# Performance work log

Measured on AMD Instinct MI355X. Metric: run time of the kernel, lower is better.

## Reference

```python
import jax, jax.numpy as jnp
import numpy as np

B, S, D = 4, 2048, 1024
H, HD = 16, 64
TAU = HD ** -0.5
N_MASKED = 256  # last keys masked (padding)


def setup_inputs() -> dict:
    key = jax.random.key(0)
    ks = jax.random.split(key, 8)
    sc = 0.02
    mask = jnp.zeros((B, 1, 1, S), dtype=bool).at[..., S - N_MASKED:].set(True)
    return {
        "q": jax.random.normal(ks[0], (B, S, D), dtype=jnp.float32),
        "k": jax.random.normal(ks[1], (B, S, D), dtype=jnp.float32),
        "v": jax.random.normal(ks[2], (B, S, D), dtype=jnp.float32),
        "mask": mask,
        "Wq": jax.random.normal(ks[3], (D, H * HD), dtype=jnp.float32) * sc,
        "bq": jnp.zeros((H * HD,), dtype=jnp.float32),
        "Wk": jax.random.normal(ks[4], (D, H * HD), dtype=jnp.float32) * sc,
        "bk": jnp.zeros((H * HD,), dtype=jnp.float32),
        "Wv": jax.random.normal(ks[5], (D, H * HD), dtype=jnp.float32) * sc,
        "bv": jnp.zeros((H * HD,), dtype=jnp.float32),
        "Wo": jax.random.normal(ks[6], (H * HD, D), dtype=jnp.float32) * sc,
        "bo": jnp.zeros((D,), dtype=jnp.float32),
    }


def reference(q, k, v, mask, Wq, bq, Wk, bk, Wv, bv, Wo, bo):
    # projections: [..., s, D] -> [..., s, H, HD]
    qh = (q @ Wq + bq).reshape(*q.shape[:-1], H, HD)
    kh = (k @ Wk + bk).reshape(*k.shape[:-1], H, HD)
    vh = (v @ Wv + bv).reshape(*v.shape[:-1], H, HD)
    # scores: [B, H, Q, K]
    attn = jnp.einsum('bqhd,bkhd->bhqk', qh, kh) * TAU
    attn = jnp.where(mask, -jnp.inf, attn)  # masked_fill(mask, -inf)
    # dropout(p=0) before softmax is identity
    p = jax.nn.softmax(attn, axis=-1)
    out = jnp.einsum('bhqk,bkhd->bqhd', p, vh).reshape(*q.shape[:-1], H * HD)
    return out @ Wo + bo  # [B, S, D]
```

## Files before the change

kernel.cpp:

```cpp
#include <hip/hip_runtime.h>
#include <hip/hip_fp16.h>
#include <cstdint>
#include <cstddef>

#define B_  4
#define S_  2048
#define D_  1024
#define H_  16
#define HD_ 64
#define TAU_ 0.125f
#define QSCALE_ 0.18033688011112042f

typedef _Float16 f16;
typedef __attribute__((ext_vector_type(8)))  _Float16 f16x8;
typedef __attribute__((ext_vector_type(4)))  _Float16 f16x4;
typedef __attribute__((ext_vector_type(2)))  __fp16   fp16x2_b;
typedef __attribute__((ext_vector_type(4)))  float    f32x4;
typedef __attribute__((ext_vector_type(16))) float    f32x16;
typedef __attribute__((ext_vector_type(2)))  unsigned u32x2;

__device__ __forceinline__ void gload_lds16(const f16* g, f16* l) {
    __builtin_amdgcn_global_load_lds(
        (const __attribute__((address_space(1))) unsigned int*)g,
        (__attribute__((address_space(3)))       unsigned int*)l,
        16, 0, 0);
}

__device__ __forceinline__ unsigned pkh(float a, float b) {
    fp16x2_b h = __builtin_amdgcn_cvt_pkrtz(a, b);
    return __builtin_bit_cast(unsigned, h);
}

__device__ __forceinline__ float exp2_hw(float x) {
    float r;
    asm("v_exp_f32 %0, %1" : "=v"(r) : "v"(x));
    return r;
}

__device__ __forceinline__ float max3f(float a, float b, float c) {
    float r;
    asm("v_max3_f32 %0, %1, %2, %3" : "=v"(r) : "v"(a), "v"(b), "v"(c));
    return r;
}

__device__ __forceinline__ float pair_max(float x) {
    unsigned xu = __builtin_bit_cast(unsigned, x);
    u32x2 r = __builtin_amdgcn_permlane32_swap(xu, xu, false, false);
    return fmaxf(__builtin_bit_cast(float, r[0]), __builtin_bit_cast(float, r[1]));
}
__device__ __forceinline__ float pair_sum(float x) {
    unsigned xu = __builtin_bit_cast(unsigned, x);
    u32x2 r = __builtin_amdgcn_permlane32_swap(xu, xu, false, false);
    return __builtin_bit_cast(float, r[0]) + __builtin_bit_cast(float, r[1]);
}

__global__ __launch_bounds__(256) void mask_norm_kernel(
    const unsigned char* __restrict__ mp, unsigned char* __restrict__ nm,
    float* __restrict__ mf)
{
    __shared__ int flags[3];
    const int tid = threadIdx.x;
    if (tid < 3) flags[tid] = 0;
    __syncthreads();
    int loc0 = 0, loc1 = 0, loc2 = 0;
    for (int i = 0; i < 32; ++i) {
        int off = tid * 32 + i;
        unsigned char v = mp[off];
        if (v) {
            int m = off & 3;
            if (m == 0) loc0 = 1;
            else if (m == 1) loc1 = 1;
            else loc2 = 1;
        }
    }
    if (loc0) atomicOr(&flags[0], 1);
    if (loc1) atomicOr(&flags[1], 1);
    if (loc2) atomicOr(&flags[2], 1);
    __syncthreads();
    const int mode = flags[1] ? 0 : (flags[2] ? 2 : (flags[0] ? 1 : 0));
    for (int i = 0; i < 32; ++i) {
        int idx = tid * 32 + i;
        unsigned char r;
        if (mode == 0)      r = mp[idx] ? 1 : 0;
        else if (mode == 1) r = ((const int*)mp)[idx] ? 1 : 0;
        else                r = (((const float*)mp)[idx] != 0.f) ? 1 : 0;
        nm[idx] = r;
        mf[idx] = r ? -1e30f : 0.f;
    }
}

__global__ __launch_bounds__(256) void wconv_kernel(
    const float* __restrict__ W0, const float* __restrict__ W1,
    const float* __restrict__ W2, const float* __restrict__ W3,
    f16* __restrict__ Wt)
{
    __shared__ float T[64][65];
    const int z = blockIdx.z;
    const float* W = (z == 0) ? W0 : (z == 1) ? W1 : (z == 2) ? W2 : W3;
    f16* out = Wt + (size_t)z * D_ * D_;
    const int n0 = blockIdx.x * 64, k0 = blockIdx.y * 64;
    const int tid = threadIdx.x;
    for (int j = 0; j < 4; ++j) {
        int idx = j * 256 + tid;
        int r = idx >> 4, c4 = idx & 15;
        float4 v = *(const float4*)&W[(size_t)(k0 + r) * D_ + n0 + c4 * 4];
        T[r][c4 * 4 + 0] = v.x; T[r][c4 * 4 + 1] = v.y;
        T[r][c4 * 4 + 2] = v.z; T[r][c4 * 4 + 3] = v.w;
    }
    __syncthreads();
    for (int j = 0; j < 16; ++j) {
        int idx = j * 256 + tid;
        int nl = idx >> 6, kl = idx & 63;
        out[(size_t)(n0 + nl) * D_ + k0 + kl] = (f16)T[kl][nl];
    }
}

__global__ __launch_bounds__(256) void f32to16_kernel(
    const float* __restrict__ a0, const float* __restrict__ a1,
    const float* __restrict__ a2, f16* __restrict__ o0,
    f16* __restrict__ o1, f16* __restrict__ o2)
{
    const int z = blockIdx.y;
    const float* a = (z == 0) ? a0 : (z == 1) ? a1 : a2;
    f16* o = (z == 0) ? o0 : (z == 1) ? o1 : o2;
    const int N4 = (B_ * S_ * D_) / 4;
    for (int i = blockIdx.x * 256 + threadIdx.x; i < N4; i += gridDim.x * 256) {
        float4 v = ((const float4*)a)[i];
        f16x4 h;
        h[0] = (f16)v.x; h[1] = (f16)v.y; h[2] = (f16)v.z; h[3] = (f16)v.w;
        ((f16x4*)o)[i] = h;
    }
}

template <bool A16>
__device__ __forceinline__ void gemm_body(
    const void* __restrict__ Ap, const f16* __restrict__ Wt,
    const float* __restrict__ bias, void* __restrict__ Cp,
    int m0, int n0, float oscale, int outmode)
{
    __shared__ __align__(16) f16 Al[128 * 64];
    __shared__ __align__(16) f16 Bl[128 * 64];
    const int tid = threadIdx.x, lane = tid & 63, wid = tid >> 6;
    const int wm = (wid >> 1) * 64, wn = (wid & 1) * 64;
    const int g = lane >> 4, c = lane & 15;

    f32x4 acc[4][4] = {};

    for (int kt = 0; kt < 16; ++kt) {
        const int k0 = kt * 64;
        for (int i = 0; i < 4; ++i) {
            int ch  = wid * 4 + i;
            int row = ch * 8 + (lane >> 3);
            int ls  = (lane & 7) ^ (row & 7);
            gload_lds16(Wt + (size_t)(n0 + row) * 1024 + k0 + ls * 8,
                        Bl + ch * 512);
        }
        if (A16) {
            const f16* A = (const f16*)Ap;
            for (int i = 0; i < 4; ++i) {
                int ch  = wid * 4 + i;
                int row = ch * 8 + (lane >> 3);
                int ls  = (lane & 7) ^ (row & 7);
                gload_lds16(A + (size_t)(m0 + row) * 1024 + k0 + ls * 8,
                            Al + ch * 512);
            }
        } else {
            const float* A = (const float*)Ap;
            for (int j = 0; j < 8; ++j) {
                int idx = j * 256 + tid;
                int row = idx >> 4, c4 = idx & 15;
                float4 v = *(const float4*)&A[(size_t)(m0 + row) * 1024 + k0 + c4 * 4];
                f16x4 h;
                h[0] = (f16)v.x; h[1] = (f16)v.y; h[2] = (f16)v.z; h[3] = (f16)v.w;
                int ps = (c4 >> 1) ^ (row & 7);
                *(f16x4*)&Al[row * 64 + ps * 8 + (c4 & 1) * 4] = h;
            }
        }
        __syncthreads();
        for (int kc = 0; kc < 2; ++kc) {
            f16x8 af[4], bf[4];
            for (int mb = 0; mb < 4; ++mb) {
                int row = wm + mb * 16 + c;
                af[mb] = *(const f16x8*)&Al[row * 64 + ((kc * 4 + g) ^ (row & 7)) * 8];
            }
            for (int nb = 0; nb < 4; ++nb) {
                int row = wn + nb * 16 + c;
                bf[nb] = *(const f16x8*)&Bl[row * 64 + ((kc * 4 + g) ^ (row & 7)) * 8];
            }
            for (int mb = 0; mb < 4; ++mb)
                for (int nb = 0; nb < 4; ++nb)
                    acc[mb][nb] = __builtin_amdgcn_mfma_f32_16x16x32_f16(
                        af[mb], bf[nb], acc[mb][nb], 0, 0, 0);
        }
        __syncthreads();
    }
    for (int nb = 0; nb < 4; ++nb) {
        int n = n0 + wn + nb * 16 + c;
        float bv = bias[n];
        for (int mb = 0; mb < 4; ++mb)
            for (int r = 0; r < 4; ++r) {
                int m = m0 + wm + mb * 16 + g * 4 + r;
                float v = (acc[mb][nb][r] + bv) * oscale;
                if (outmode == 1) {
                    ((f16*)Cp)[(((size_t)(m >> 11) * H_ + (n >> 6)) * HD_ + (n & 63)) * S_ + (m & 2047)] = (f16)v;
                } else if (outmode == 0) {
                    ((f16*)Cp)[(size_t)m * 1024 + n] = (f16)v;
                } else {
                    ((float*)Cp)[(size_t)m * 1024 + n] = v;
                }
            }
    }
}

__global__ __launch_bounds__(256) void gemm_qkv16_kernel(
    const f16* __restrict__ qf, const f16* __restrict__ kf,
    const f16* __restrict__ vf, const f16* __restrict__ Wt,
    const float* __restrict__ bq, const float* __restrict__ bk,
    const float* __restrict__ bv, f16* __restrict__ outbase)
{
    const int z = blockIdx.z;
    const f16* A    = (z == 0) ? qf : (z == 1) ? kf : vf;
    const float* bi = (z == 0) ? bq : (z == 1) ? bk : bv;
    gemm_body<true>(A, Wt + (size_t)z * D_ * D_, bi,
                    outbase + (size_t)z * S_ * B_ * D_,
                    blockIdx.x * 128, blockIdx.y * 128,
                    z == 0 ? QSCALE_ : 1.f, z == 2 ? 1 : 0);
}

__global__ __launch_bounds__(256) void gemm_qkv32_kernel(
    const float* __restrict__ q, const float* __restrict__ k,
    const float* __restrict__ v, const f16* __restrict__ Wt,
    const float* __restrict__ bq, const float* __restrict__ bk,
    const float* __restrict__ bv, f16* __restrict__ outbase)
{
    const int z = blockIdx.z;
    const float* A  = (z == 0) ? q  : (z == 1) ? k  : v;
    const float* bi = (z == 0) ? bq : (z == 1) ? bk : bv;
    gemm_body<false>(A, Wt + (size_t)z * D_ * D_, bi,
                     outbase + (size_t)z * S_ * B_ * D_,
                     blockIdx.x * 128, blockIdx.y * 128,
                     z == 0 ? QSCALE_ : 1.f, z == 2 ? 1 : 0);
}

__global__ __launch_bounds__(256) void gemm_out_kernel(
    const f16* __restrict__ Oh, const f16* __restrict__ WtO,
    const float* __restrict__ bo, float* __restrict__ out)
{
    gemm_body<true>(Oh, WtO, bo, out, blockIdx.x * 128, blockIdx.y * 128, 1.f, 2);
}

__global__ __launch_bounds__(256, 2) void attn_kernel(
    const f16* __restrict__ qh, const f16* __restrict__ kh,
    const f16* __restrict__ vt, const unsigned char* __restrict__ maskp,
    const float* __restrict__ maskf, f16* __restrict__ Oh)
{
    __shared__ __align__(16) f16 Kl[2][128 * 64];
    __shared__ __align__(16) f16 VTl[2][64 * 128];
    const int tid = threadIdx.x, lane = tid & 63, wid = tid >> 6;
    const int ql = lane & 31, hi = lane >> 5;
    const int lg = ((blockIdx.x & 7) << 7) + (blockIdx.x >> 3);
    const int h = (lg >> 4) & 15, b = lg >> 8;
    const int q0 = (lg & 15) * 128 + wid * 32;

    const unsigned char* mrow = maskp + (size_t)b * S_;
    const float* mfrow = maskf + (size_t)b * S_;
    const size_t kbase  = (size_t)b * S_ * D_ + (size_t)h * HD_;
    const size_t vtbase = ((size_t)b * H_ + h) * (size_t)HD_ * S_;

    unsigned live = 0, part = 0;
    for (int t = 0; t < 16; ++t) {
        unsigned long long b0 = __ballot(mrow[t * 128 + lane] != 0);
        unsigned long long b1 = __ballot(mrow[t * 128 + 64 + lane] != 0);
        if (b0 != ~0ull || b1 != ~0ull) {
            live |= 1u << t;
            if (b0 | b1) part |= 1u << t;
        }
    }

    f16x8 qf[4];
    {
        const f16* qrow = qh + ((size_t)(b * S_ + q0 + ql) * H_ + h) * HD_;
        #pragma unroll
        for (int dc = 0; dc < 4; ++dc)
            qf[dc] = *(const f16x8*)&qrow[dc * 16 + hi * 8];
    }

    float m_ = -1e30f, l_ = 0.f;
    f32x16 accO[2] = {};

    auto stage = [&](int kv0, int bb) {
        #pragma unroll
        for (int i = 0; i < 4; ++i) {
            int ch  = wid * 4 + i;
            int row = ch * 8 + (lane >> 3);
            int ls  = (lane & 7) ^ (row & 7);
            gload_lds16(kh + kbase + (size_t)(kv0 + row) * D_ + ls * 8,
                        &Kl[bb][ch * 512]);
            int hdr = ch * 4 + (lane >> 4);
            int vs  = (lane & 15) ^ ((hdr & 7) << 1);
            gload_lds16(vt + vtbase + (size_t)hdr * S_ + kv0 + vs * 8,
                        &VTl[bb][ch * 512]);
        }
    };

    if (live) {
        int t = __builtin_ctz(live);
        stage(t * 128, 0);
        __syncthreads();
        int cur = 0;
        for (;;) {
            unsigned rem = live & (0xFFFFFFFEu << t);
            int tn = rem ? __builtin_ctz(rem) : 32;
            if (tn < 32) stage(tn * 128, cur ^ 1);

            const int kv0 = t * 128;
            const f16* Kb = &Kl[cur][0];
            const f16* Vb = &VTl[cur][0];

            f32x16 sacc[4] = {};
            __builtin_amdgcn_s_setprio(1);
            #pragma unroll
            for (int ks = 0; ks < 4; ++ks) {
                const int key = ks * 32 + ql;
                #pragma unroll
                for (int dc = 0; dc < 4; ++dc) {
                    int slot = (dc * 2 + hi) ^ (key & 7);
                    f16x8 kf = *(const f16x8*)&Kb[key * 64 + slot * 8];
                    sacc[ks] = __builtin_amdgcn_mfma_f32_32x32x16_f16(
                        kf, qf[dc], sacc[ks], 0, 0, 0);
                }
            }
            __builtin_amdgcn_s_setprio(0);
            if (part & (1u << t)) {
                #pragma unroll
                for (int ks = 0; ks < 4; ++ks)
                    #pragma unroll
                    for (int r = 0; r < 16; ++r) {
                        int key = kv0 + ks * 32 + (r & 3) + 8 * (r >> 2) + 4 * hi;
                        sacc[ks][r] += mfrow[key];
                    }
            }
            float mx;
            {
                float m0 = max3f(sacc[0][0], sacc[0][1], sacc[0][2]);
                float m1 = max3f(sacc[1][0], sacc[1][1], sacc[1][2]);
                float m2 = max3f(sacc[2][0], sacc[2][1], sacc[2][2]);
                float m3 = max3f(sacc[3][0], sacc[3][1], sacc[3][2]);
                #pragma unroll
                for (int r = 3; r < 15; r += 2) {
                    m0 = max3f(m0, sacc[0][r], sacc[0][r + 1]);
                    m1 = max3f(m1, sacc[1][r], sacc[1][r + 1]);
                    m2 = max3f(m2, sacc[2][r], sacc[2][r + 1]);
                    m3 = max3f(m3, sacc[3][r], sacc[3][r + 1]);
                }
                m0 = fmaxf(m0, sacc[0][15]); m1 = fmaxf(m1, sacc[1][15]);
                m2 = fmaxf(m2, sacc[2][15]); m3 = fmaxf(m3, sacc[3][15]);
                mx = max3f(m0, m1, m2);
                mx = fmaxf(mx, m3);
            }
            mx = pair_max(mx);
            if (__ballot(mx > m_ + 8.f)) {
                float mnew = fmaxf(m_, mx);
                float alpha = exp2_hw(m_ - mnew);
                m_ = mnew;
                l_ *= alpha;
                #pragma unroll
                for (int blk = 0; blk < 2; ++blk)
                    #pragma unroll
                    for (int r = 0; r < 16; ++r) accO[blk][r] *= alpha;
            }
            float ts = 0.f;
            #pragma unroll
            for (int ks = 0; ks < 4; ++ks)
                #pragma unroll
                for (int r = 0; r < 16; ++r) {
                    float p = exp2_hw(sacc[ks][r] - m_);
                    sacc[ks][r] = p;
                    ts += p;
                }
            l_ += pair_sum(ts);

            #pragma unroll
            for (int ks = 0; ks < 4; ++ks) {
                unsigned Pq[4][2];
                #pragma unroll
                for (int j = 0; j < 4; ++j) {
                    Pq[j][0] = pkh(sacc[ks][4 * j + 0], sacc[ks][4 * j + 1]);
                    Pq[j][1] = pkh(sacc[ks][4 * j + 2], sacc[ks][4 * j + 3]);
                }
                #pragma unroll
                for (int kc = 0; kc < 2; ++kc) {
                    union { f16x8 v; unsigned u[4]; } pf;
                    u32x2 s0 = __builtin_amdgcn_permlane32_swap(Pq[2 * kc][0], Pq[2 * kc + 1][0], false, false);
                    u32x2 s1 = __builtin_amdgcn_permlane32_swap(Pq[2 * kc][1], Pq[2 * kc + 1][1], false, false);
                    pf.u[0] = s0[0]; pf.u[2] = s0[1];
                    pf.u[1] = s1[0]; pf.u[3] = s1[1];
                    const int s = ks * 2 + kc;
                    __builtin_amdgcn_s_setprio(1);
                    #pragma unroll
                    for (int blk = 0; blk < 2; ++blk) {
                        int hd = blk * 32 + ql;
                        int slot = (s * 2 + hi) ^ ((hd & 7) << 1);
                        f16x8 vtf = *(const f16x8*)&Vb[hd * 128 + slot * 8];
                        accO[blk] = __builtin_amdgcn_mfma_f32_32x32x16_f16(
                            vtf, pf.v, accO[blk], 0, 0, 0);
                    }
                    __builtin_amdgcn_s_setprio(0);
                }
            }
            __syncthreads();
            cur ^= 1;
            if (tn == 32) break;
            t = tn;
        }
    }
    const float invl = (l_ > 0.f) ? 1.f / l_ : 0.f;
    f16* orow = Oh + ((size_t)(b * S_ + q0 + ql) * H_ + h) * HD_;
    #pragma unroll
    for (int blk = 0; blk < 2; ++blk)
        #pragma unroll
        for (int j = 0; j < 4; ++j) {
            f16x4 o;
            #pragma unroll
            for (int tt = 0; tt < 4; ++tt)
                o[tt] = (f16)(accO[blk][4 * j + tt] * invl);
            *(f16x4*)&orow[blk * 32 + 4 * hi + 8 * j] = o;
        }
}

extern "C" void kernel_launch(void* const* d_in, const int* in_sizes, int n_in,
                              void* d_out, int out_size, void* d_ws, size_t ws_size,
                              hipStream_t stream)
{
    const float* q    = (const float*)d_in[0];
    const float* k    = (const float*)d_in[1];
    const float* v    = (const float*)d_in[2];
    const unsigned char* mask = (const unsigned char*)d_in[3];
    const float* Wq   = (const float*)d_in[4];
    const float* bq   = (const float*)d_in[5];
    const float* Wk   = (const float*)d_in[6];
    const float* bk   = (const float*)d_in[7];
    const float* Wv   = (const float*)d_in[8];
    const float* bv   = (const float*)d_in[9];
    const float* Wo   = (const float*)d_in[10];
    const float* bo   = (const float*)d_in[11];
    float* out        = (float*)d_out;

    char* ws = (char*)d_ws;
    const size_t MB = 1048576;
    f16* Wt  = (f16*)ws;
    f16* qh  = (f16*)(ws + 8 * MB);
    f16* khp = (f16*)(ws + 24 * MB);
    f16* vtp = (f16*)(ws + 40 * MB);
    f16* Ohp = (f16*)(ws + 56 * MB);
    unsigned char* nm = (unsigned char*)(ws + 72 * MB);
    float* mf = (float*)(ws + 72 * MB + 8192);
    f16* qf16 = (f16*)(ws + 76 * MB);
    f16* kf16 = (f16*)(ws + 92 * MB);
    f16* vf16 = (f16*)(ws + 108 * MB);
    const bool use16 = ws_size >= 124 * MB;

    mask_norm_kernel<<<1, 256, 0, stream>>>(mask, nm, mf);
    wconv_kernel<<<dim3(16, 16, 4), 256, 0, stream>>>(Wq, Wk, Wv, Wo, Wt);
    if (use16) {
        f32to16_kernel<<<dim3(1024, 3), 256, 0, stream>>>(q, k, v, qf16, kf16, vf16);
        gemm_qkv16_kernel<<<dim3(64, 8, 3), 256, 0, stream>>>(
            qf16, kf16, vf16, Wt, bq, bk, bv, qh);
    } else {
        gemm_qkv32_kernel<<<dim3(64, 8, 3), 256, 0, stream>>>(
            q, k, v, Wt, bq, bk, bv, qh);
    }
    attn_kernel<<<1024, 256, 0, stream>>>(qh, khp, vtp, nm, mf, Ohp);
    gemm_out_kernel<<<dim3(64, 8), 256, 0, stream>>>(Ohp, Wt + (size_t)3 * D_ * D_, bo, out);
}
```

Baseline: 243.5 us.

## Load fp32 activations directly to LDS and convert in QKV GEMM

Drops the separate fp32-to-fp16 conversion pass over q, k and v. The QKV projection GEMM now loads fp32 activation tiles straight into shared memory with async global-to-LDS copies, using a 16-way XOR swizzle, and converts them to fp16 when reading MFMA fragments. This avoids writing and re-reading about 48 MB of fp16 intermediates and saves a kernel launch. In exchange the A tile doubles in LDS, each tile is converted redundantly by the two wave columns, and more A bytes are read per GEMM tile.

```diff
diff --git a/kernel.cpp b/kernel.cpp
--- a/kernel.cpp
+++ b/kernel.cpp
@@ -19,7 +19,7 @@
 typedef __attribute__((ext_vector_type(16))) float    f32x16;
 typedef __attribute__((ext_vector_type(2)))  unsigned u32x2;
 
-__device__ __forceinline__ void gload_lds16(const f16* g, f16* l) {
+__device__ __forceinline__ void gload_lds16(const void* g, void* l) {
     __builtin_amdgcn_global_load_lds(
         (const __attribute__((address_space(1))) unsigned int*)g,
         (__attribute__((address_space(3)))       unsigned int*)l,
@@ -115,31 +115,22 @@
     }
 }
 
-__global__ __launch_bounds__(256) void f32to16_kernel(
-    const float* __restrict__ a0, const float* __restrict__ a1,
-    const float* __restrict__ a2, f16* __restrict__ o0,
-    f16* __restrict__ o1, f16* __restrict__ o2)
-{
-    const int z = blockIdx.y;
-    const float* a = (z == 0) ? a0 : (z == 1) ? a1 : a2;
-    f16* o = (z == 0) ? o0 : (z == 1) ? o1 : o2;
-    const int N4 = (B_ * S_ * D_) / 4;
-    for (int i = blockIdx.x * 256 + threadIdx.x; i < N4; i += gridDim.x * 256) {
-        float4 v = ((const float4*)a)[i];
-        f16x4 h;
-        h[0] = (f16)v.x; h[1] = (f16)v.y; h[2] = (f16)v.z; h[3] = (f16)v.w;
-        ((f16x4*)o)[i] = h;
-    }
-}
-
-template <bool A16>
-__device__ __forceinline__ void gemm_body(
-    const void* __restrict__ Ap, const f16* __restrict__ Wt,
-    const float* __restrict__ bias, void* __restrict__ Cp,
-    int m0, int n0, float oscale, int outmode)
-{
-    __shared__ __align__(16) f16 Al[128 * 64];
-    __shared__ __align__(16) f16 Bl[128 * 64];
+__global__ __launch_bounds__(256) void gemm_qkvf_kernel(
+    const float* __restrict__ q, const float* __restrict__ k,
+    const float* __restrict__ v, const f16* __restrict__ Wt,
+    const float* __restrict__ bq, const float* __restrict__ bk,
+    const float* __restrict__ bv, f16* __restrict__ outbase)
+{
+    __shared__ __align__(16) float Al[128 * 64];
+    __shared__ __align__(16) f16  Bl[128 * 64];
+    const int z = blockIdx.z;
+    const float* A  = (z == 0) ? q  : (z == 1) ? k  : v;
+    const float* bi = (z == 0) ? bq : (z == 1) ? bk : bv;
+    const f16*  W   = Wt + (size_t)z * D_ * D_;
+    f16* Cp         = outbase + (size_t)z * S_ * B_ * D_;
+    const float oscale = (z == 0) ? QSCALE_ : 1.f;
+    const int outmode  = (z == 2) ? 1 : 0;
+    const int m0 = blockIdx.x * 128, n0 = blockIdx.y * 128;
     const int tid = threadIdx.x, lane = tid & 63, wid = tid >> 6;
     const int wm = (wid >> 1) * 64, wn = (wid & 1) * 64;
     const int g = lane >> 4, c = lane & 15;
@@ -152,29 +143,81 @@
             int ch  = wid * 4 + i;
             int row = ch * 8 + (lane >> 3);
             int ls  = (lane & 7) ^ (row & 7);
-            gload_lds16(Wt + (size_t)(n0 + row) * 1024 + k0 + ls * 8,
+            gload_lds16(W + (size_t)(n0 + row) * 1024 + k0 + ls * 8,
                         Bl + ch * 512);
         }
-        if (A16) {
-            const f16* A = (const f16*)Ap;
-            for (int i = 0; i < 4; ++i) {
-                int ch  = wid * 4 + i;
-                int row = ch * 8 + (lane >> 3);
-                int ls  = (lane & 7) ^ (row & 7);
-                gload_lds16(A + (size_t)(m0 + row) * 1024 + k0 + ls * 8,
-                            Al + ch * 512);
-            }
-        } else {
-            const float* A = (const float*)Ap;
-            for (int j = 0; j < 8; ++j) {
-                int idx = j * 256 + tid;
-                int row = idx >> 4, c4 = idx & 15;
-                float4 v = *(const float4*)&A[(size_t)(m0 + row) * 1024 + k0 + c4 * 4];
-                f16x4 h;
-                h[0] = (f16)v.x; h[1] = (f16)v.y; h[2] = (f16)v.z; h[3] = (f16)v.w;
-                int ps = (c4 >> 1) ^ (row & 7);
-                *(f16x4*)&Al[row * 64 + ps * 8 + (c4 & 1) * 4] = h;
-            }
+        for (int i = 0; i < 8; ++i) {
+            int ch  = wid * 8 + i;
+            int row = ch * 4 + (lane >> 4);
+            int ls  = (lane & 15) ^ (row & 15);
+            gload_lds16(A + (size_t)(m0 + row) * 1024 + k0 + ls * 4,
+                        Al + ch * 256);
+        }
+        __syncthreads();
+        for (int kc = 0; kc < 2; ++kc) {
+            f16x8 af[4], bf[4];
+            for (int mb = 0; mb < 4; ++mb) {
+                int row = wm + mb * 16 + c;
+                int sl  = kc * 8 + g * 2;
+                f32x4 a0 = *(const f32x4*)&Al[row * 64 + ((sl)     ^ (row & 15)) * 4];
+                f32x4 a1 = *(const f32x4*)&Al[row * 64 + ((sl + 1) ^ (row & 15)) * 4];
+                f16x8 hfr;
+                hfr[0] = (f16)a0[0]; hfr[1] = (f16)a0[1];
+                hfr[2] = (f16)a0[2]; hfr[3] = (f16)a0[3];
+                hfr[4] = (f16)a1[0]; hfr[5] = (f16)a1[1];
+                hfr[6] = (f16)a1[2]; hfr[7] = (f16)a1[3];
+                af[mb] = hfr;
+            }
+            for (int nb = 0; nb < 4; ++nb) {
+                int row = wn + nb * 16 + c;
+                bf[nb] = *(const f16x8*)&Bl[row * 64 + ((kc * 4 + g) ^ (row & 7)) * 8];
+            }
+            for (int mb = 0; mb < 4; ++mb)
+                for (int nb = 0; nb < 4; ++nb)
+                    acc[mb][nb] = __builtin_amdgcn_mfma_f32_16x16x32_f16(
+                        af[mb], bf[nb], acc[mb][nb], 0, 0, 0);
+        }
+        __syncthreads();
+    }
+    for (int nb = 0; nb < 4; ++nb) {
+        int n = n0 + wn + nb * 16 + c;
+        float bv2 = bi[n];
+        for (int mb = 0; mb < 4; ++mb)
+            for (int r = 0; r < 4; ++r) {
+                int m = m0 + wm + mb * 16 + g * 4 + r;
+                float val = (acc[mb][nb][r] + bv2) * oscale;
+                if (outmode == 1) {
+                    Cp[(((size_t)(m >> 11) * H_ + (n >> 6)) * HD_ + (n & 63)) * S_ + (m & 2047)] = (f16)val;
+                } else {
+                    Cp[(size_t)m * 1024 + n] = (f16)val;
+                }
+            }
+    }
+}
+
+__global__ __launch_bounds__(256) void gemm_out_kernel(
+    const f16* __restrict__ Oh, const f16* __restrict__ WtO,
+    const float* __restrict__ bo, float* __restrict__ out)
+{
+    __shared__ __align__(16) f16 Al[128 * 64];
+    __shared__ __align__(16) f16 Bl[128 * 64];
+    const int m0 = blockIdx.x * 128, n0 = blockIdx.y * 128;
+    const int tid = threadIdx.x, lane = tid & 63, wid = tid >> 6;
+    const int wm = (wid >> 1) * 64, wn = (wid & 1) * 64;
+    const int g = lane >> 4, c = lane & 15;
+
+    f32x4 acc[4][4] = {};
+
+    for (int kt = 0; kt < 16; ++kt) {
+        const int k0 = kt * 64;
+        for (int i = 0; i < 4; ++i) {
+            int ch  = wid * 4 + i;
+            int row = ch * 8 + (lane >> 3);
+            int ls  = (lane & 7) ^ (row & 7);
+            gload_lds16(WtO + (size_t)(n0 + row) * 1024 + k0 + ls * 8,
+                        Bl + ch * 512);
+            gload_lds16(Oh + (size_t)(m0 + row) * 1024 + k0 + ls * 8,
+                        Al + ch * 512);
         }
         __syncthreads();
         for (int kc = 0; kc < 2; ++kc) {
@@ -196,57 +239,13 @@
     }
     for (int nb = 0; nb < 4; ++nb) {
         int n = n0 + wn + nb * 16 + c;
-        float bv = bias[n];
+        float bv = bo[n];
         for (int mb = 0; mb < 4; ++mb)
             for (int r = 0; r < 4; ++r) {
                 int m = m0 + wm + mb * 16 + g * 4 + r;
-                float v = (acc[mb][nb][r] + bv) * oscale;
-                if (outmode == 1) {
-                    ((f16*)Cp)[(((size_t)(m >> 11) * H_ + (n >> 6)) * HD_ + (n & 63)) * S_ + (m & 2047)] = (f16)v;
-                } else if (outmode == 0) {
-                    ((f16*)Cp)[(size_t)m * 1024 + n] = (f16)v;
-                } else {
-                    ((float*)Cp)[(size_t)m * 1024 + n] = v;
-                }
-            }
-    }
-}
-
-__global__ __launch_bounds__(256) void gemm_qkv16_kernel(
-    const f16* __restrict__ qf, const f16* __restrict__ kf,
-    const f16* __restrict__ vf, const f16* __restrict__ Wt,
-    const float* __restrict__ bq, const float* __restrict__ bk,
-    const float* __restrict__ bv, f16* __restrict__ outbase)
-{
-    const int z = blockIdx.z;
-    const f16* A    = (z == 0) ? qf : (z == 1) ? kf : vf;
-    const float* bi = (z == 0) ? bq : (z == 1) ? bk : bv;
-    gemm_body<true>(A, Wt + (size_t)z * D_ * D_, bi,
-                    outbase + (size_t)z * S_ * B_ * D_,
-                    blockIdx.x * 128, blockIdx.y * 128,
-                    z == 0 ? QSCALE_ : 1.f, z == 2 ? 1 : 0);
-}
-
-__global__ __launch_bounds__(256) void gemm_qkv32_kernel(
-    const float* __restrict__ q, const float* __restrict__ k,
-    const float* __restrict__ v, const f16* __restrict__ Wt,
-    const float* __restrict__ bq, const float* __restrict__ bk,
-    const float* __restrict__ bv, f16* __restrict__ outbase)
-{
-    const int z = blockIdx.z;
-    const float* A  = (z == 0) ? q  : (z == 1) ? k  : v;
-    const float* bi = (z == 0) ? bq : (z == 1) ? bk : bv;
-    gemm_body<false>(A, Wt + (size_t)z * D_ * D_, bi,
-                     outbase + (size_t)z * S_ * B_ * D_,
-                     blockIdx.x * 128, blockIdx.y * 128,
-                     z == 0 ? QSCALE_ : 1.f, z == 2 ? 1 : 0);
-}
-
-__global__ __launch_bounds__(256) void gemm_out_kernel(
-    const f16* __restrict__ Oh, const f16* __restrict__ WtO,
-    const float* __restrict__ bo, float* __restrict__ out)
-{
-    gemm_body<true>(Oh, WtO, bo, out, blockIdx.x * 128, blockIdx.y * 128, 1.f, 2);
+                out[(size_t)m * 1024 + n] = acc[mb][nb][r] + bv;
+            }
+    }
 }
 
 __global__ __launch_bounds__(256, 2) void attn_kernel(
@@ -455,21 +454,10 @@
     f16* Ohp = (f16*)(ws + 56 * MB);
     unsigned char* nm = (unsigned char*)(ws + 72 * MB);
     float* mf = (float*)(ws + 72 * MB + 8192);
-    f16* qf16 = (f16*)(ws + 76 * MB);
-    f16* kf16 = (f16*)(ws + 92 * MB);
-    f16* vf16 = (f16*)(ws + 108 * MB);
-    const bool use16 = ws_size >= 124 * MB;
 
     mask_norm_kernel<<<1, 256, 0, stream>>>(mask, nm, mf);
     wconv_kernel<<<dim3(16, 16, 4), 256, 0, stream>>>(Wq, Wk, Wv, Wo, Wt);
-    if (use16) {
-        f32to16_kernel<<<dim3(1024, 3), 256, 0, stream>>>(q, k, v, qf16, kf16, vf16);
-        gemm_qkv16_kernel<<<dim3(64, 8, 3), 256, 0, stream>>>(
-            qf16, kf16, vf16, Wt, bq, bk, bv, qh);
-    } else {
-        gemm_qkv32_kernel<<<dim3(64, 8, 3), 256, 0, stream>>>(
-            q, k, v, Wt, bq, bk, bv, qh);
-    }
+    gemm_qkvf_kernel<<<dim3(64, 8, 3), 256, 0, stream>>>(q, k, v, Wt, bq, bk, bv, qh);
     attn_kernel<<<1024, 256, 0, stream>>>(qh, khp, vtp, nm, mf, Ohp);
     gemm_out_kernel<<<dim3(64, 8), 256, 0, stream>>>(Ohp, Wt + (size_t)3 * D_ * D_, bo, out);
 }
```

After: 232.7 us. -4.4%, faster.
